# Kernel optimization log

Hardware: AMD Instinct MI355X
Metric: run time of the kernel (lower is better)

The kernel has to match this reference:

```python
import jax, jax.numpy as jnp
import numpy as np

N_HEADS, N_KV_HEADS, HEAD_DIM = 32, 8, 128
N_REP = N_HEADS // N_KV_HEADS


def apply_rope(x, cos, sin):
    # x: [B, H, T, D]; cos/sin: [T, D/2]. Interleaved complex rotation (LLaMA style).
    x1 = x[..., 0::2]
    x2 = x[..., 1::2]
    c = cos[None, None, :, :]
    s = sin[None, None, :, :]
    r1 = x1 * c - x2 * s
    r2 = x1 * s + x2 * c
    return jnp.stack([r1, r2], axis=-1).reshape(x.shape)


def setup_inputs() -> dict:
    key = jax.random.key(0)
    ks = jax.random.split(key, 7)
    B, T, D = 1, 2048, 4096
    sc = 0.02
    return {
        "x": jax.random.normal(ks[0], (B, T, D), jnp.float32),
        "cos": jnp.cos(jax.random.normal(ks[1], (T, HEAD_DIM // 2), jnp.float32)),
        "sin": jnp.sin(jax.random.normal(ks[1], (T, HEAD_DIM // 2), jnp.float32)),
        "wq": jax.random.normal(ks[2], (D, D), jnp.float32) * sc,
        "wk": jax.random.normal(ks[3], (N_KV_HEADS * HEAD_DIM, D), jnp.float32) * sc,
        "wv": jax.random.normal(ks[4], (N_KV_HEADS * HEAD_DIM, D), jnp.float32) * sc,
        "wo": jax.random.normal(ks[5], (D, D), jnp.float32) * sc,
    }


def reference(x, cos, sin, wq, wk, wv, wo):
    B, T, _ = x.shape
    # QKV projections (nn.Linear: y = x @ W^T)
    q = (x @ wq.T).reshape(B, T, N_HEADS, HEAD_DIM).transpose(0, 2, 1, 3)
    k = (x @ wk.T).reshape(B, T, N_KV_HEADS, HEAD_DIM).transpose(0, 2, 1, 3)
    v = (x @ wv.T).reshape(B, T, N_KV_HEADS, HEAD_DIM).transpose(0, 2, 1, 3)
    # RoPE on q, k
    q = apply_rope(q, cos[:T], sin[:T])
    k = apply_rope(k, cos[:T], sin[:T])
    # GQA: repeat_interleave kv heads along head dim
    if N_REP > 1:
        k = jnp.repeat(k, N_REP, axis=1)
        v = jnp.repeat(v, N_REP, axis=1)
    # causal SDPA
    scale = 1.0 / jnp.sqrt(jnp.float32(HEAD_DIM))
    scores = jnp.einsum("bhqd,bhkd->bhqk", q, k) * scale
    causal = jnp.tril(jnp.ones((T, T), dtype=bool))
    scores = jnp.where(causal[None, None], scores, jnp.finfo(scores.dtype).min)
    attn = jax.nn.softmax(scores, axis=-1)
    y = jnp.einsum("bhqk,bhkd->bhqd", attn, v)
    y = y.transpose(0, 2, 1, 3).reshape(B, T, -1)
    return y @ wo.T
```

## Files before the change

### kernel.cpp

```cpp
#include <hip/hip_runtime.h>
#include <stdint.h>

typedef unsigned short ushort_t;
typedef __attribute__((ext_vector_type(8))) __bf16 bf16x8;
typedef __attribute__((ext_vector_type(4))) float f32x4;

#define MFMA16(a, b, c) __builtin_amdgcn_mfma_f32_16x16x32_bf16((a), (b), (c), 0, 0, 0)

__device__ __forceinline__ ushort_t f2bf(float f) {
    unsigned u = __float_as_uint(f);
    u += 0x7fffu + ((u >> 16) & 1u);
    return (ushort_t)(u >> 16);
}

typedef __attribute__((address_space(1))) const unsigned char g_u8;
typedef __attribute__((address_space(3))) unsigned char l_u8;
__device__ __forceinline__ void gload16(const void* g, void* l) {
    __builtin_amdgcn_global_load_lds((g_u8*)g, (l_u8*)(unsigned int)(uintptr_t)l, 16, 0, 0);
}

__global__ __launch_bounds__(256) void cast_multi(const float* __restrict__ x,
                                                  const float* __restrict__ wq,
                                                  const float* __restrict__ wk,
                                                  const float* __restrict__ wv,
                                                  ushort_t* __restrict__ xb,
                                                  ushort_t* __restrict__ wqb,
                                                  ushort_t* __restrict__ wkb,
                                                  ushort_t* __restrict__ wvb) {
    int i = blockIdx.x * 256 + threadIdx.x;
    const float* in; ushort_t* out; int off;
    if (i < 2097152)      { in = x;  out = xb;  off = i; }
    else if (i < 6291456) { in = wq; out = wqb; off = i - 2097152; }
    else if (i < 7340032) { in = wk; out = wkb; off = i - 6291456; }
    else                  { in = wv; out = wvb; off = i - 7340032; }
    float4 v = ((const float4*)in)[off];
    ushort4 o;
    o.x = f2bf(v.x); o.y = f2bf(v.y); o.z = f2bf(v.z); o.w = f2bf(v.w);
    ((ushort4*)out)[off] = o;
}

__global__ __launch_bounds__(256) void cast_f32_bf16(const float* __restrict__ in,
                                                     ushort_t* __restrict__ out, int n4) {
    int i = blockIdx.x * 256 + threadIdx.x;
    if (i < n4) {
        float4 v = ((const float4*)in)[i];
        ushort4 o;
        o.x = f2bf(v.x); o.y = f2bf(v.y); o.z = f2bf(v.z); o.w = f2bf(v.w);
        ((ushort4*)out)[i] = o;
    }
}

#define GEMM_K_LOOP(Aarr, Barr, KDIM)                                                   \
    const ushort_t* aptr[4]; const ushort_t* bptr[4]; int ldsoff[4];                    \
    _Pragma("unroll")                                                                   \
    for (int p = 0; p < 4; p++) {                                                       \
        int s = p * 256 + tid;                                                          \
        int row = s >> 3;                                                               \
        int kc = (s & 7) ^ (row & 7);                                                   \
        aptr[p] = Aarr + (size_t)(bm + row) * (KDIM) + kc * 8;                          \
        bptr[p] = Barr + (size_t)(bn + row) * (KDIM) + kc * 8;                          \
        ldsoff[p] = s * 8;                                                              \
    }                                                                                   \
    const int r7 = l16 & 7;                                                             \
    for (int k0 = 0; k0 < (KDIM); k0 += 64) {                                           \
        _Pragma("unroll")                                                               \
        for (int p = 0; p < 4; p++) {                                                   \
            gload16(aptr[p] + k0, As + ldsoff[p]);                                      \
            gload16(bptr[p] + k0, Bs + ldsoff[p]);                                      \
        }                                                                               \
        __syncthreads();                                                                \
        _Pragma("unroll")                                                               \
        for (int ks2 = 0; ks2 < 2; ks2++) {                                             \
            bf16x8 af[4], bfr[4];                                                       \
            _Pragma("unroll")                                                           \
            for (int i = 0; i < 4; i++)                                                 \
                af[i] = *(const bf16x8*)(&As[(wm + i * 16 + l16) * 64 +                 \
                                             (((ks2 * 4 + quad) ^ r7) << 3)]);          \
            _Pragma("unroll")                                                           \
            for (int j = 0; j < 4; j++)                                                 \
                bfr[j] = *(const bf16x8*)(&Bs[(wn + j * 16 + l16) * 64 +                \
                                              (((ks2 * 4 + quad) ^ r7) << 3)]);         \
            _Pragma("unroll")                                                           \
            for (int i = 0; i < 4; i++)                                                 \
                _Pragma("unroll")                                                       \
                for (int j = 0; j < 4; j++)                                             \
                    acc[i][j] = MFMA16(af[i], bfr[j], acc[i][j]);                       \
        }                                                                               \
        __syncthreads();                                                                \
    }

__global__ __launch_bounds__(256) void gemm_qkv(const ushort_t* __restrict__ A,
                                                const ushort_t* __restrict__ Wq,
                                                const ushort_t* __restrict__ Wk,
                                                const ushort_t* __restrict__ Wv,
                                                ushort_t* __restrict__ Qo,
                                                ushort_t* __restrict__ Ko,
                                                ushort_t* __restrict__ VtO,
                                                const float* __restrict__ cosp,
                                                const float* __restrict__ sinp) {
    const int by = blockIdx.y;
    const ushort_t* B;
    int region, bn;
    if (by < 32)      { region = 0; B = Wq; bn = by * 128; }
    else if (by < 40) { region = 1; B = Wk; bn = (by - 32) * 128; }
    else              { region = 2; B = Wv; bn = (by - 40) * 128; }
    const int bm = blockIdx.x * 128;

    __shared__ __align__(16) ushort_t As[128 * 64];
    __shared__ __align__(16) ushort_t Bs[128 * 64];
    const int tid = threadIdx.x;
    const int w = tid >> 6, lane = tid & 63;
    const int quad = lane >> 4, l16 = lane & 15;
    const int wm = (w >> 1) * 64, wn = (w & 1) * 64;
    f32x4 acc[4][4] = {};

    GEMM_K_LOOP(A, B, 4096)

    const float qscale = 0.08838834764831845f;
    if (region < 2) {
        ushort_t* C = (region == 0) ? Qo : Ko;
        const int Nc = (region == 0) ? 4096 : 1024;
        const float scl = (region == 0) ? qscale : 1.0f;
#pragma unroll
        for (int i = 0; i < 4; i++)
#pragma unroll
            for (int j = 0; j < 4; j++) {
                const int col = bn + wn + j * 16 + l16;
                const int pj = (col & 127) >> 1;
#pragma unroll
                for (int r = 0; r < 4; r++) {
                    const int row = bm + wm + i * 16 + quad * 4 + r;
                    float v = acc[i][j][r];
                    float p = __shfl_xor(v, 1);
                    float c = cosp[row * 64 + pj], s = sinp[row * 64 + pj];
                    float res = (col & 1) ? fmaf(p, s, v * c)
                                          : (v * c - p * s);
                    C[(size_t)row * Nc + col] = f2bf(res * scl);
                }
            }
    } else {
#pragma unroll
        for (int i = 0; i < 4; i++) {
            const int rowb = bm + wm + i * 16 + quad * 4;
#pragma unroll
            for (int j = 0; j < 4; j++) {
                const int col = bn + wn + j * 16 + l16;
                ushort4 pk;
                pk.x = f2bf(acc[i][j][0]); pk.y = f2bf(acc[i][j][1]);
                pk.z = f2bf(acc[i][j][2]); pk.w = f2bf(acc[i][j][3]);
                *(ushort4*)(VtO + (size_t)col * 2048 + rowb) = pk;
            }
        }
    }
}

__global__ __launch_bounds__(256) void gemm_bt(const ushort_t* __restrict__ A,
                                               const ushort_t* __restrict__ B,
                                               float* __restrict__ C,
                                               int M, int N, int K) {
    const int bm = blockIdx.x * 128, bn = blockIdx.y * 128;
    __shared__ __align__(16) ushort_t As[128 * 64];
    __shared__ __align__(16) ushort_t Bs[128 * 64];
    const int tid = threadIdx.x;
    const int w = tid >> 6, lane = tid & 63;
    const int quad = lane >> 4, l16 = lane & 15;
    const int wm = (w >> 1) * 64, wn = (w & 1) * 64;
    f32x4 acc[4][4] = {};

    GEMM_K_LOOP(A, B, K)

#pragma unroll
    for (int i = 0; i < 4; i++)
#pragma unroll
        for (int j = 0; j < 4; j++)
#pragma unroll
            for (int r = 0; r < 4; r++) {
                int row = bm + wm + i * 16 + quad * 4 + r;
                int col = bn + wn + j * 16 + l16;
                C[(size_t)row * N + col] = acc[i][j][r];
            }
}

__global__ __launch_bounds__(512) void flash_attn(const ushort_t* __restrict__ Q,
                                                  const ushort_t* __restrict__ Kp,
                                                  const ushort_t* __restrict__ Vt,
                                                  ushort_t* __restrict__ Y) {
    const int by = blockIdx.y;
    const int kh = by >> 1;
    const int hbase = kh * 4 + (by & 1) * 2;
    const int tid = threadIdx.x;
    const int w = tid >> 6, lane = tid & 63;
    const int wh = w >> 2, wr = w & 3;
    const int h = hbase + wh;
    const int quad = lane >> 4, l16 = lane & 15;

    __shared__ __align__(16) ushort_t Ks[64 * 136];
    __shared__ __align__(16) ushort_t VtS[128 * 88];
    __shared__ __align__(16) ushort_t Ps[8 * 16 * 88];

    bf16x8 ones;
#pragma unroll
    for (int e = 0; e < 8; e++) ((ushort_t*)&ones)[e] = 0x3F80;

#pragma unroll 1
    for (int phase = 0; phase < 2; phase++) {
        const int qt = (phase == 0) ? blockIdx.x : 31 - blockIdx.x;

        bf16x8 qf[4];
        {
            const ushort_t* qrow = Q + (size_t)(qt * 64 + wr * 16 + l16) * 4096 + h * 128 + quad * 8;
#pragma unroll
            for (int ks = 0; ks < 4; ks++) qf[ks] = *(const bf16x8*)(qrow + ks * 32);
        }

        f32x4 o[8] = {};
        f32x4 lacc = {};
        float m_i[4];
#pragma unroll
        for (int r = 0; r < 4; r++) m_i[r] = -1e30f;

        const int ntiles = qt + 1;
        for (int j = 0; j < ntiles; j++) {
            const int t0 = j * 64;
            {
#pragma unroll
                for (int p = 0; p < 2; p++) {
                    int ck = p * 512 + tid;
                    int r = ck >> 4, c = (ck & 15) * 8;
                    uint4 d = *(const uint4*)(Kp + (size_t)(t0 + r) * 1024 + kh * 128 + c);
                    *(uint4*)(&Ks[r * 136 + c]) = d;
                }
            }
            {
#pragma unroll
                for (int p = 0; p < 2; p++) {
                    int ck = p * 512 + tid;
                    int d = ck >> 3, c = (ck & 7) * 8;
                    uint4 v = *(const uint4*)(Vt + (size_t)(kh * 128 + d) * 2048 + t0 + c);
                    *(uint4*)(&VtS[d * 88 + c]) = v;
                }
            }
            __syncthreads();

            f32x4 s[4] = {};
#pragma unroll
            for (int ct = 0; ct < 4; ct++)
#pragma unroll
                for (int ks = 0; ks < 4; ks++) {
                    bf16x8 kf = *(const bf16x8*)(&Ks[(ct * 16 + l16) * 136 + ks * 32 + quad * 8]);
                    s[ct] = MFMA16(qf[ks], kf, s[ct]);
                }

            if (j == qt) {
#pragma unroll
                for (int ct = 0; ct < 4; ct++)
#pragma unroll
                    for (int r = 0; r < 4; r++) {
                        int rg = wr * 16 + quad * 4 + r;
                        int cg = ct * 16 + l16;
                        if (cg > rg) s[ct][r] = -1e30f;
                    }
            }

            float alpha[4];
#pragma unroll
            for (int r = 0; r < 4; r++) {
                float v = fmaxf(fmaxf(s[0][r], s[1][r]), fmaxf(s[2][r], s[3][r]));
                v = fmaxf(v, __shfl_xor(v, 1));
                v = fmaxf(v, __shfl_xor(v, 2));
                v = fmaxf(v, __shfl_xor(v, 4));
                v = fmaxf(v, __shfl_xor(v, 8));
                float mn = fmaxf(m_i[r], v);
                alpha[r] = __expf(m_i[r] - mn);
                m_i[r] = mn;
            }
#pragma unroll
            for (int ct = 0; ct < 4; ct++)
#pragma unroll
                for (int r = 0; r < 4; r++)
                    s[ct][r] = __expf(s[ct][r] - m_i[r]);
#pragma unroll
            for (int n = 0; n < 8; n++)
#pragma unroll
                for (int r = 0; r < 4; r++) o[n][r] *= alpha[r];
#pragma unroll
            for (int r = 0; r < 4; r++) lacc[r] *= alpha[r];

#pragma unroll
            for (int ct = 0; ct < 4; ct++)
#pragma unroll
                for (int r = 0; r < 4; r++)
                    Ps[w * 1408 + (quad * 4 + r) * 88 + ct * 16 + l16] = f2bf(s[ct][r]);
            __threadfence_block();

#pragma unroll
            for (int ks2 = 0; ks2 < 2; ks2++) {
                bf16x8 pf = *(const bf16x8*)(&Ps[w * 1408 + l16 * 88 + ks2 * 32 + quad * 8]);
                lacc = MFMA16(pf, ones, lacc);
#pragma unroll
                for (int n = 0; n < 8; n++) {
                    bf16x8 vf = *(const bf16x8*)(&VtS[(n * 16 + l16) * 88 + ks2 * 32 + quad * 8]);
                    o[n] = MFMA16(pf, vf, o[n]);
                }
            }
            __syncthreads();
        }

        float inv[4];
#pragma unroll
        for (int r = 0; r < 4; r++) inv[r] = 1.0f / lacc[r];
#pragma unroll
        for (int n = 0; n < 8; n++)
#pragma unroll
            for (int r = 0; r < 4; r++) {
                int row = qt * 64 + wr * 16 + quad * 4 + r;
                int col = h * 128 + n * 16 + l16;
                Y[(size_t)row * 4096 + col] = f2bf(o[n][r] * inv[r]);
            }
    }
}

extern "C" void kernel_launch(void* const* d_in, const int* in_sizes, int n_in,
                              void* d_out, int out_size, void* d_ws, size_t ws_size,
                              hipStream_t stream) {
    const float* x    = (const float*)d_in[0];
    const float* cosp = (const float*)d_in[1];
    const float* sinp = (const float*)d_in[2];
    const float* wq   = (const float*)d_in[3];
    const float* wk   = (const float*)d_in[4];
    const float* wv   = (const float*)d_in[5];
    const float* wo   = (const float*)d_in[6];
    float* out = (float*)d_out;

    ushort_t* xb   = (ushort_t*)d_ws;
    ushort_t* qb   = xb  + (size_t)2048 * 4096;
    ushort_t* yb   = qb  + (size_t)2048 * 4096;
    ushort_t* kb   = yb  + (size_t)2048 * 4096;
    ushort_t* vtb  = kb  + (size_t)2048 * 1024;
    ushort_t* wkb  = vtb + (size_t)1024 * 2048;
    ushort_t* wvb  = wkb + (size_t)1024 * 4096;
    ushort_t* wbig = wvb + (size_t)1024 * 4096;

    cast_multi<<<32768, 256, 0, stream>>>(x, wq, wk, wv, xb, wbig, wkb, wvb);

    {
        dim3 g(16, 48, 1);
        gemm_qkv<<<g, 256, 0, stream>>>(xb, wbig, wkb, wvb, qb, kb, vtb, cosp, sinp);
    }

    {
        dim3 g(16, 16, 1);
        flash_attn<<<g, 512, 0, stream>>>(qb, kb, vtb, yb);
    }

    cast_f32_bf16<<<16384, 256, 0, stream>>>(wo, wbig, 4096 * 4096 / 4);
    {
        dim3 g(16, 32, 1);
        gemm_bt<<<g, 256, 0, stream>>>(yb, wbig, out, 2048, 4096, 4096);
    }
}
```

Baseline: 530.9 us.

## Switch GEMMs to 32x32 MFMA, fold wo cast into QKV GEMM, reshape attention grid

The GEMM inner loop moves from 16x16x32 to 32x32x16 bf16 MFMA with 2x2 f32x16 accumulators, which cuts LDS fragment reads per MFMA. Epilogues are remapped to the 32x32 output layout, and launch bounds gain an occupancy hint of 3. When the workspace is large enough, the wo fp32-to-bf16 cast runs as extra blocks of the QKV GEMM launch instead of as its own kernel. Flash attention now uses one head per 256-thread block across 32 head blocks instead of two heads per 512-thread block, trading shared K/V tiles for more, smaller blocks.

Result: faster. 472.2 us (-11.1%).

```diff
diff --git a/kernel.cpp b/kernel.cpp
--- a/kernel.cpp
+++ b/kernel.cpp
@@ -4,8 +4,10 @@
 typedef unsigned short ushort_t;
 typedef __attribute__((ext_vector_type(8))) __bf16 bf16x8;
 typedef __attribute__((ext_vector_type(4))) float f32x4;
+typedef __attribute__((ext_vector_type(16))) float f32x16;
 
 #define MFMA16(a, b, c) __builtin_amdgcn_mfma_f32_16x16x32_bf16((a), (b), (c), 0, 0, 0)
+#define MFMA32(a, b, c) __builtin_amdgcn_mfma_f32_32x32x16_bf16((a), (b), (c), 0, 0, 0)
 
 __device__ __forceinline__ ushort_t f2bf(float f) {
     unsigned u = __float_as_uint(f);
@@ -61,7 +63,7 @@
         bptr[p] = Barr + (size_t)(bn + row) * (KDIM) + kc * 8;                          \
         ldsoff[p] = s * 8;                                                              \
     }                                                                                   \
-    const int r7 = l16 & 7;                                                             \
+    const int l32 = lane & 31, hi = lane >> 5, r7 = l32 & 7;                            \
     for (int k0 = 0; k0 < (KDIM); k0 += 64) {                                           \
         _Pragma("unroll")                                                               \
         for (int p = 0; p < 4; p++) {                                                   \
@@ -70,35 +72,49 @@
         }                                                                               \
         __syncthreads();                                                                \
         _Pragma("unroll")                                                               \
-        for (int ks2 = 0; ks2 < 2; ks2++) {                                             \
-            bf16x8 af[4], bfr[4];                                                       \
-            _Pragma("unroll")                                                           \
-            for (int i = 0; i < 4; i++)                                                 \
-                af[i] = *(const bf16x8*)(&As[(wm + i * 16 + l16) * 64 +                 \
-                                             (((ks2 * 4 + quad) ^ r7) << 3)]);          \
-            _Pragma("unroll")                                                           \
-            for (int j = 0; j < 4; j++)                                                 \
-                bfr[j] = *(const bf16x8*)(&Bs[(wn + j * 16 + l16) * 64 +                \
-                                              (((ks2 * 4 + quad) ^ r7) << 3)]);         \
-            _Pragma("unroll")                                                           \
-            for (int i = 0; i < 4; i++)                                                 \
-                _Pragma("unroll")                                                       \
-                for (int j = 0; j < 4; j++)                                             \
-                    acc[i][j] = MFMA16(af[i], bfr[j], acc[i][j]);                       \
+        for (int ks = 0; ks < 4; ks++) {                                                \
+            const int swz = ((ks * 2 + hi) ^ r7) << 3;                                  \
+            bf16x8 a0 = *(const bf16x8*)(&As[(wm + l32) * 64 + swz]);                   \
+            bf16x8 a1 = *(const bf16x8*)(&As[(wm + 32 + l32) * 64 + swz]);              \
+            bf16x8 b0 = *(const bf16x8*)(&Bs[(wn + l32) * 64 + swz]);                   \
+            bf16x8 b1 = *(const bf16x8*)(&Bs[(wn + 32 + l32) * 64 + swz]);              \
+            acc[0][0] = MFMA32(a0, b0, acc[0][0]);                                      \
+            acc[0][1] = MFMA32(a0, b1, acc[0][1]);                                      \
+            acc[1][0] = MFMA32(a1, b0, acc[1][0]);                                      \
+            acc[1][1] = MFMA32(a1, b1, acc[1][1]);                                      \
         }                                                                               \
         __syncthreads();                                                                \
     }
 
-__global__ __launch_bounds__(256) void gemm_qkv(const ushort_t* __restrict__ A,
-                                                const ushort_t* __restrict__ Wq,
-                                                const ushort_t* __restrict__ Wk,
-                                                const ushort_t* __restrict__ Wv,
-                                                ushort_t* __restrict__ Qo,
-                                                ushort_t* __restrict__ Ko,
-                                                ushort_t* __restrict__ VtO,
-                                                const float* __restrict__ cosp,
-                                                const float* __restrict__ sinp) {
+__global__ __launch_bounds__(256, 3) void gemm_qkv(const ushort_t* __restrict__ A,
+                                                   const ushort_t* __restrict__ Wq,
+                                                   const ushort_t* __restrict__ Wk,
+                                                   const ushort_t* __restrict__ Wv,
+                                                   ushort_t* __restrict__ Qo,
+                                                   ushort_t* __restrict__ Ko,
+                                                   ushort_t* __restrict__ VtO,
+                                                   const float* __restrict__ cosp,
+                                                   const float* __restrict__ sinp,
+                                                   const float* __restrict__ wo,
+                                                   ushort_t* __restrict__ wob) {
     const int by = blockIdx.y;
+    const int tid = threadIdx.x;
+
+    if (by >= 48) {
+        const int ci = (by - 48) * gridDim.x + blockIdx.x;
+        const float4* src = (const float4*)wo;
+        ushort4* dst = (ushort4*)wob;
+        int base = ci * 4096 + tid;
+#pragma unroll
+        for (int p = 0; p < 16; p++) {
+            float4 v = src[base + p * 256];
+            ushort4 o;
+            o.x = f2bf(v.x); o.y = f2bf(v.y); o.z = f2bf(v.z); o.w = f2bf(v.w);
+            dst[base + p * 256] = o;
+        }
+        return;
+    }
+
     const ushort_t* B;
     int region, bn;
     if (by < 32)      { region = 0; B = Wq; bn = by * 128; }
@@ -108,11 +124,9 @@
 
     __shared__ __align__(16) ushort_t As[128 * 64];
     __shared__ __align__(16) ushort_t Bs[128 * 64];
-    const int tid = threadIdx.x;
     const int w = tid >> 6, lane = tid & 63;
-    const int quad = lane >> 4, l16 = lane & 15;
     const int wm = (w >> 1) * 64, wn = (w & 1) * 64;
-    f32x4 acc[4][4] = {};
+    f32x16 acc[2][2] = {};
 
     GEMM_K_LOOP(A, B, 4096)
 
@@ -122,14 +136,14 @@
         const int Nc = (region == 0) ? 4096 : 1024;
         const float scl = (region == 0) ? qscale : 1.0f;
 #pragma unroll
-        for (int i = 0; i < 4; i++)
-#pragma unroll
-            for (int j = 0; j < 4; j++) {
-                const int col = bn + wn + j * 16 + l16;
+        for (int i = 0; i < 2; i++)
+#pragma unroll
+            for (int j = 0; j < 2; j++) {
+                const int col = bn + wn + j * 32 + l32;
                 const int pj = (col & 127) >> 1;
 #pragma unroll
-                for (int r = 0; r < 4; r++) {
-                    const int row = bm + wm + i * 16 + quad * 4 + r;
+                for (int r = 0; r < 16; r++) {
+                    const int row = bm + wm + i * 32 + (r & 3) + 8 * (r >> 2) + 4 * hi;
                     float v = acc[i][j][r];
                     float p = __shfl_xor(v, 1);
                     float c = cosp[row * 64 + pj], s = sinp[row * 64 + pj];
@@ -140,63 +154,63 @@
             }
     } else {
 #pragma unroll
-        for (int i = 0; i < 4; i++) {
-            const int rowb = bm + wm + i * 16 + quad * 4;
-#pragma unroll
-            for (int j = 0; j < 4; j++) {
-                const int col = bn + wn + j * 16 + l16;
-                ushort4 pk;
-                pk.x = f2bf(acc[i][j][0]); pk.y = f2bf(acc[i][j][1]);
-                pk.z = f2bf(acc[i][j][2]); pk.w = f2bf(acc[i][j][3]);
-                *(ushort4*)(VtO + (size_t)col * 2048 + rowb) = pk;
-            }
-        }
-    }
-}
-
-__global__ __launch_bounds__(256) void gemm_bt(const ushort_t* __restrict__ A,
-                                               const ushort_t* __restrict__ B,
-                                               float* __restrict__ C,
-                                               int M, int N, int K) {
+        for (int i = 0; i < 2; i++)
+#pragma unroll
+            for (int j = 0; j < 2; j++) {
+                const int col = bn + wn + j * 32 + l32;
+#pragma unroll
+                for (int g = 0; g < 4; g++) {
+                    const int rowb = bm + wm + i * 32 + g * 8 + 4 * hi;
+                    ushort4 pk;
+                    pk.x = f2bf(acc[i][j][g * 4 + 0]);
+                    pk.y = f2bf(acc[i][j][g * 4 + 1]);
+                    pk.z = f2bf(acc[i][j][g * 4 + 2]);
+                    pk.w = f2bf(acc[i][j][g * 4 + 3]);
+                    *(ushort4*)(VtO + (size_t)col * 2048 + rowb) = pk;
+                }
+            }
+    }
+}
+
+__global__ __launch_bounds__(256, 3) void gemm_bt(const ushort_t* __restrict__ A,
+                                                  const ushort_t* __restrict__ B,
+                                                  float* __restrict__ C,
+                                                  int M, int N, int K) {
     const int bm = blockIdx.x * 128, bn = blockIdx.y * 128;
     __shared__ __align__(16) ushort_t As[128 * 64];
     __shared__ __align__(16) ushort_t Bs[128 * 64];
     const int tid = threadIdx.x;
     const int w = tid >> 6, lane = tid & 63;
-    const int quad = lane >> 4, l16 = lane & 15;
     const int wm = (w >> 1) * 64, wn = (w & 1) * 64;
-    f32x4 acc[4][4] = {};
+    f32x16 acc[2][2] = {};
 
     GEMM_K_LOOP(A, B, K)
 
 #pragma unroll
-    for (int i = 0; i < 4; i++)
-#pragma unroll
-        for (int j = 0; j < 4; j++)
-#pragma unroll
-            for (int r = 0; r < 4; r++) {
-                int row = bm + wm + i * 16 + quad * 4 + r;
-                int col = bn + wn + j * 16 + l16;
+    for (int i = 0; i < 2; i++)
+#pragma unroll
+        for (int j = 0; j < 2; j++) {
+            const int col = bn + wn + j * 32 + l32;
+#pragma unroll
+            for (int r = 0; r < 16; r++) {
+                const int row = bm + wm + i * 32 + (r & 3) + 8 * (r >> 2) + 4 * hi;
                 C[(size_t)row * N + col] = acc[i][j][r];
             }
-}
-
-__global__ __launch_bounds__(512) void flash_attn(const ushort_t* __restrict__ Q,
+        }
+}
+
+__global__ __launch_bounds__(256) void flash_attn(const ushort_t* __restrict__ Q,
                                                   const ushort_t* __restrict__ Kp,
                                                   const ushort_t* __restrict__ Vt,
                                                   ushort_t* __restrict__ Y) {
-    const int by = blockIdx.y;
-    const int kh = by >> 1;
-    const int hbase = kh * 4 + (by & 1) * 2;
+    const int h = blockIdx.y, kh = h >> 2;
     const int tid = threadIdx.x;
     const int w = tid >> 6, lane = tid & 63;
-    const int wh = w >> 2, wr = w & 3;
-    const int h = hbase + wh;
     const int quad = lane >> 4, l16 = lane & 15;
 
     __shared__ __align__(16) ushort_t Ks[64 * 136];
     __shared__ __align__(16) ushort_t VtS[128 * 88];
-    __shared__ __align__(16) ushort_t Ps[8 * 16 * 88];
+    __shared__ __align__(16) ushort_t Ps[4 * 16 * 88];
 
     bf16x8 ones;
 #pragma unroll
@@ -208,7 +222,7 @@
 
         bf16x8 qf[4];
         {
-            const ushort_t* qrow = Q + (size_t)(qt * 64 + wr * 16 + l16) * 4096 + h * 128 + quad * 8;
+            const ushort_t* qrow = Q + (size_t)(qt * 64 + w * 16 + l16) * 4096 + h * 128 + quad * 8;
 #pragma unroll
             for (int ks = 0; ks < 4; ks++) qf[ks] = *(const bf16x8*)(qrow + ks * 32);
         }
@@ -224,8 +238,8 @@
             const int t0 = j * 64;
             {
 #pragma unroll
-                for (int p = 0; p < 2; p++) {
-                    int ck = p * 512 + tid;
+                for (int p = 0; p < 4; p++) {
+                    int ck = p * 256 + tid;
                     int r = ck >> 4, c = (ck & 15) * 8;
                     uint4 d = *(const uint4*)(Kp + (size_t)(t0 + r) * 1024 + kh * 128 + c);
                     *(uint4*)(&Ks[r * 136 + c]) = d;
@@ -233,8 +247,8 @@
             }
             {
 #pragma unroll
-                for (int p = 0; p < 2; p++) {
-                    int ck = p * 512 + tid;
+                for (int p = 0; p < 4; p++) {
+                    int ck = p * 256 + tid;
                     int d = ck >> 3, c = (ck & 7) * 8;
                     uint4 v = *(const uint4*)(Vt + (size_t)(kh * 128 + d) * 2048 + t0 + c);
                     *(uint4*)(&VtS[d * 88 + c]) = v;
@@ -256,7 +270,7 @@
                 for (int ct = 0; ct < 4; ct++)
 #pragma unroll
                     for (int r = 0; r < 4; r++) {
-                        int rg = wr * 16 + quad * 4 + r;
+                        int rg = w * 16 + quad * 4 + r;
                         int cg = ct * 16 + l16;
                         if (cg > rg) s[ct][r] = -1e30f;
                     }
@@ -313,7 +327,7 @@
         for (int n = 0; n < 8; n++)
 #pragma unroll
             for (int r = 0; r < 4; r++) {
-                int row = qt * 64 + wr * 16 + quad * 4 + r;
+                int row = qt * 64 + w * 16 + quad * 4 + r;
                 int col = h * 128 + n * 16 + l16;
                 Y[(size_t)row * 4096 + col] = f2bf(o[n][r] * inv[r]);
             }
@@ -340,22 +354,28 @@
     ushort_t* wkb  = vtb + (size_t)1024 * 2048;
     ushort_t* wvb  = wkb + (size_t)1024 * 4096;
     ushort_t* wbig = wvb + (size_t)1024 * 4096;
+    ushort_t* wob  = wbig + (size_t)4096 * 4096;
+    const size_t need_fused = (size_t)(wob + (size_t)4096 * 4096 - xb) * sizeof(ushort_t);
+    const bool fuse_wo = ws_size >= need_fused;
 
     cast_multi<<<32768, 256, 0, stream>>>(x, wq, wk, wv, xb, wbig, wkb, wvb);
 
     {
-        dim3 g(16, 48, 1);
-        gemm_qkv<<<g, 256, 0, stream>>>(xb, wbig, wkb, wvb, qb, kb, vtb, cosp, sinp);
-    }
-
-    {
-        dim3 g(16, 16, 1);
-        flash_attn<<<g, 512, 0, stream>>>(qb, kb, vtb, yb);
-    }
-
-    cast_f32_bf16<<<16384, 256, 0, stream>>>(wo, wbig, 4096 * 4096 / 4);
+        dim3 g(16, fuse_wo ? 112 : 48, 1);
+        gemm_qkv<<<g, 256, 0, stream>>>(xb, wbig, wkb, wvb, qb, kb, vtb, cosp, sinp,
+                                        wo, fuse_wo ? wob : wbig);
+    }
+
     {
         dim3 g(16, 32, 1);
-        gemm_bt<<<g, 256, 0, stream>>>(yb, wbig, out, 2048, 4096, 4096);
-    }
-}
+        flash_attn<<<g, 256, 0, stream>>>(qb, kb, vtb, yb);
+    }
+
+    const ushort_t* wo_b = fuse_wo ? wob : wbig;
+    if (!fuse_wo)
+        cast_f32_bf16<<<16384, 256, 0, stream>>>(wo, wbig, 4096 * 4096 / 4);
+    {
+        dim3 g(16, 32, 1);
+        gemm_bt<<<g, 256, 0, stream>>>(yb, wo_b, out, 2048, 4096, 4096);
+    }
+}
```
